# Performance work log

Measured on AMD Instinct MI355X. Metric: run time of the kernel, lower is better.

Reference implementation:

```python
import jax, jax.numpy as jnp
import numpy as np

N_NODES = 40000            # num nodes (maybe_num_nodes)
E = 2_560_000              # input edges
SENTINEL = N_NODES * N_NODES  # key for masked-out edges; sorts last; fits int32 (1.6e9 < 2^31)


def setup_inputs() -> dict:
    key = jax.random.key(0)
    k1, k2 = jax.random.split(key)
    edge_index = jax.random.randint(k1, (2, E), 0, N_NODES, dtype=jnp.int32)
    edge_attr = jax.random.uniform(k2, (E,), dtype=jnp.float32)
    t = jnp.full((1,), 0.5, dtype=jnp.float32)  # learnable threshold parameter
    return {"edge_index": edge_index, "edge_attr": edge_attr, "t": t}


def reference(edge_index, edge_attr, t):
    """Threshold mask -> symmetrize -> coalesce (sort by (row,col), sum duplicates).

    JAX has static shapes, so compaction is expressed as masking: dropped edges get
    key=SENTINEL (sorts last) and attr contribution 0. Returns padded outputs of
    fixed size 2E plus the count of valid (unique, kept) edges. Invalid slots have
    edge_index == -1 and edge_attr == 0.
    """
    row, col = edge_index[0], edge_index[1]
    mask = edge_attr <= t[0]                      # [E] bool
    # symmetrize: stack (row,col) and (col,row), duplicate attrs  -> [2E]
    r2 = jnp.concatenate([row, col])
    c2 = jnp.concatenate([col, row])
    a2 = jnp.concatenate([edge_attr, edge_attr])
    m2 = jnp.concatenate([mask, mask])
    # coalesce: linearize key = row*N + col, sort, segment-sum duplicates
    key = jnp.where(m2, r2 * N_NODES + c2, SENTINEL)   # [2E] int32
    order = jnp.argsort(key)
    key_s = key[order]
    a_s = jnp.where(m2, a2, 0.0)[order]
    E2 = key_s.shape[0]
    new_seg = jnp.concatenate([jnp.ones((1,), bool), key_s[1:] != key_s[:-1]])
    seg = jnp.cumsum(new_seg.astype(jnp.int32)) - 1    # segment id per sorted edge
    vals = jax.ops.segment_sum(a_s, seg, num_segments=E2, indices_are_sorted=True)
    uk = jnp.full((E2,), SENTINEL, dtype=key_s.dtype).at[seg].set(key_s)
    valid = uk < SENTINEL
    out_row = jnp.where(valid, uk // N_NODES, -1)
    out_col = jnp.where(valid, uk % N_NODES, -1)
    edge_index_out = jnp.stack([out_row, out_col])     # [2, 2E] padded with -1
    edge_attr_out = jnp.where(valid, vals, 0.0)        # [2E]   padded with 0
    num_edges = jnp.sum(valid.astype(jnp.int32))
    return edge_index_out, edge_attr_out, num_edges
```

## Files before the change

### kernel.cpp

```cpp
#include <hip/hip_runtime.h>
#include <stdint.h>

#define NN 40000
#define E_IN 2560000
#define E2 5120000
#define NFINE 2500
#define NSB 20
#define SB_SHIFT 11
#define FINES_PER_SB 128
#define P2_TILES 17
#define P2_TILE 8192
#define SBCAP 135168
#define CAPB 1280
#define CSTR 16
#define P1_BLOCKS 625
#define P1_THREADS 1024
#define OF_BLOCKS 625
#define OF_ITERS 8

typedef unsigned long long ull;

__global__ void k_init(int* __restrict__ sbCursor, int* __restrict__ fineCursor) {
    int tid = threadIdx.x;
    for (int f = tid; f < NFINE; f += 256) fineCursor[f * CSTR] = f * CAPB;
    if (tid < NSB) sbCursor[tid * CSTR] = tid * SBCAP;
}

__global__ void __launch_bounds__(P1_THREADS) k_part1(const int* __restrict__ ei,
                                                      const float* __restrict__ ea,
                                                      const float* __restrict__ t,
                                                      int* __restrict__ sbCursor,
                                                      ull* __restrict__ pairs1) {
    __shared__ ull staged[8192];
    __shared__ int cntO[NSB * 8];
    __shared__ int off[NSB + 1], wb[NSB * 8], gbase[NSB];
    int tid = threadIdx.x;
    int oct = (tid >> 3) & 7;
    if (tid < NSB * 8) cntO[tid] = 0;
    __syncthreads();
    float t0 = t[0];
    int i0 = blockIdx.x * 4096 + tid * 4;

    float4 a4 = *(const float4*)(ea + i0);
    int4 r4 = *(const int4*)(ei + i0);
    int4 c4 = *(const int4*)(ei + E_IN + i0);
    float av[4] = {a4.x, a4.y, a4.z, a4.w};
    int rv[4] = {r4.x, r4.y, r4.z, r4.w};
    int cv[4] = {c4.x, c4.y, c4.z, c4.w};

    ull eA[4], eB[4];
    int rkA[4], rkB[4];
    bool keep[4];
#pragma unroll
    for (int k = 0; k < 4; k++) {
        keep[k] = (av[k] <= t0);
        if (keep[k]) {
            unsigned ab = __float_as_uint(av[k]);
            eA[k] = ((ull)(unsigned)rv[k] << 48) | ((ull)(unsigned)cv[k] << 32) | ab;
            eB[k] = ((ull)(unsigned)cv[k] << 48) | ((ull)(unsigned)rv[k] << 32) | ab;
            rkA[k] = atomicAdd(&cntO[((rv[k] >> SB_SHIFT) << 3) | oct], 1);
            rkB[k] = atomicAdd(&cntO[((cv[k] >> SB_SHIFT) << 3) | oct], 1);
        }
    }
    __syncthreads();
    if (tid < NSB) {
        int s = tid;
        int c[8], tot = 0;
#pragma unroll
        for (int o = 0; o < 8; o++) { c[o] = cntO[s * 8 + o]; tot += c[o]; }
        int incl = tot;
#pragma unroll
        for (int d = 1; d < 32; d <<= 1) {
            int y = __shfl_up(incl, d, 64);
            if (s >= d) incl += y;
        }
        int o0 = incl - tot;
        off[s] = o0;
        if (s == NSB - 1) off[NSB] = incl;
        int acc = o0;
#pragma unroll
        for (int o = 0; o < 8; o++) { wb[s * 8 + o] = acc; acc += c[o]; }
        gbase[s] = atomicAdd(&sbCursor[s * CSTR], tot);
    }
    __syncthreads();
#pragma unroll
    for (int k = 0; k < 4; k++) {
        if (keep[k]) {
            staged[wb[(((int)(eA[k] >> 59)) << 3) | oct] + rkA[k]] = eA[k];
            staged[wb[(((int)(eB[k] >> 59)) << 3) | oct] + rkB[k]] = eB[k];
        }
    }
    __syncthreads();
    int total = off[NSB];
    for (int i = tid; i < total; i += P1_THREADS) {
        ull e = staged[i];
        int sb = (int)(e >> 59);
        pairs1[gbase[sb] + (i - off[sb])] = e;
    }
}

__global__ void __launch_bounds__(1024) k_part2(const int* __restrict__ sbCursor,
                                                int* __restrict__ fineCursor,
                                                const ull* __restrict__ pairs1,
                                                ull* __restrict__ pairs2) {
    int sb = blockIdx.x / P2_TILES;
    int tile = blockIdx.x % P2_TILES;
    int regionBase = sb * SBCAP;
    int len = sbCursor[sb * CSTR] - regionBase;
    if (len > SBCAP) len = SBCAP;
    int start = tile * P2_TILE;
    if (start >= len) return;
    int cntT = len - start; if (cntT > P2_TILE) cntT = P2_TILE;
    const ull* src = pairs1 + regionBase + start;

    int fineFirst = sb * FINES_PER_SB;
    int nF = NFINE - fineFirst; if (nF > FINES_PER_SB) nF = FINES_PER_SB;

    __shared__ ull staged[P2_TILE];
    __shared__ int cnt[FINES_PER_SB], off[FINES_PER_SB + 1], gbase[FINES_PER_SB], wsum2[2];
    int tid = threadIdx.x;
    if (tid < FINES_PER_SB) { cnt[tid] = 0; gbase[tid] = 0; }
    __syncthreads();

    ull e[8];
    int rk[8];
#pragma unroll
    for (int k = 0; k < 8; k++) {
        int i = tid + k * 1024;
        if (i < cntT) {
            e[k] = src[i];
            rk[k] = atomicAdd(&cnt[(int)(e[k] >> 52) & 127], 1);
        }
    }
    __syncthreads();
    int x = 0, incl = 0;
    if (tid < FINES_PER_SB) {
        x = cnt[tid];
        incl = x;
        int lane = tid & 63;
#pragma unroll
        for (int d = 1; d < 64; d <<= 1) {
            int y = __shfl_up(incl, d, 64);
            if (lane >= d) incl += y;
        }
        if (lane == 63) wsum2[tid >> 6] = incl;
    }
    __syncthreads();
    if (tid == 0) { int a = wsum2[0]; wsum2[0] = 0; wsum2[1] = a; }
    __syncthreads();
    if (tid < FINES_PER_SB) {
        off[tid] = wsum2[tid >> 6] + incl - x;
        if (tid == FINES_PER_SB - 1) off[FINES_PER_SB] = wsum2[1] + incl;
        if (tid < nF) gbase[tid] = atomicAdd(&fineCursor[(fineFirst + tid) * CSTR], x);
    }
    __syncthreads();
#pragma unroll
    for (int k = 0; k < 8; k++) {
        int i = tid + k * 1024;
        if (i < cntT) staged[off[(int)(e[k] >> 52) & 127] + rk[k]] = e[k];
    }
    __syncthreads();
    int total = off[FINES_PER_SB];
    for (int i = tid; i < total; i += 1024) {
        ull v = staged[i];
        int lb = (int)(v >> 52) & 127;
        pairs2[gbase[lb] + (i - off[lb])] = v;
    }
}

__device__ __forceinline__ void ce(ull& a, ull& b) {
    ull mn = a < b ? a : b;
    ull mx = a < b ? b : a;
    a = mn; b = mx;
}
__device__ __forceinline__ void sort8(ull* v) {
    ce(v[0],v[1]); ce(v[2],v[3]); ce(v[4],v[5]); ce(v[6],v[7]);
    ce(v[0],v[2]); ce(v[1],v[3]); ce(v[4],v[6]); ce(v[5],v[7]);
    ce(v[1],v[2]); ce(v[5],v[6]);
    ce(v[0],v[4]); ce(v[1],v[5]); ce(v[2],v[6]); ce(v[3],v[7]);
    ce(v[2],v[4]); ce(v[3],v[5]);
    ce(v[1],v[2]); ce(v[3],v[4]); ce(v[5],v[6]);
}
__device__ __forceinline__ void sort16(ull* v) {
    sort8(v); sort8(v + 8);
    ce(v[0],v[8]);  ce(v[1],v[9]);  ce(v[2],v[10]); ce(v[3],v[11]);
    ce(v[4],v[12]); ce(v[5],v[13]); ce(v[6],v[14]); ce(v[7],v[15]);
    ce(v[4],v[8]);  ce(v[5],v[9]);  ce(v[6],v[10]); ce(v[7],v[11]);
    ce(v[2],v[4]);  ce(v[3],v[5]);  ce(v[6],v[8]);  ce(v[7],v[9]);  ce(v[10],v[12]); ce(v[11],v[13]);
    ce(v[1],v[2]);  ce(v[3],v[4]);  ce(v[5],v[6]);  ce(v[7],v[8]);  ce(v[9],v[10]);  ce(v[11],v[12]); ce(v[13],v[14]);
}

__global__ void __launch_bounds__(512) k_sortrows(const int* __restrict__ fineCursor,
                                                  ull* __restrict__ pairs2,
                                                  int* __restrict__ uniqueCount) {
    int b = blockIdx.x;
    int base = b * CAPB;
    int n = fineCursor[b * CSTR] - base;
    if (n > CAPB) n = CAPB;
    __shared__ ull d[CAPB];
    __shared__ int cnt[512], off[512], wsum[8], ucnt[16], ubase[16];
    int tid = threadIdx.x;
    int lane = tid & 63;
    cnt[tid] = 0;
    __syncthreads();

    ull e[3]; int rk[3], sbk[3];
#pragma unroll
    for (int k = 0; k < 3; k++) {
        int i = tid + k * 512;
        if (i < n) {
            e[k] = pairs2[base + i];
            sbk[k] = (int)(e[k] >> 43) & 511;
            rk[k] = atomicAdd(&cnt[sbk[k]], 1);
        }
    }
    __syncthreads();

    int x = cnt[tid];
    int incl = x;
#pragma unroll
    for (int dlt = 1; dlt < 64; dlt <<= 1) {
        int y = __shfl_up(incl, dlt, 64);
        if (lane >= dlt) incl += y;
    }
    if (lane == 63) wsum[tid >> 6] = incl;
    __syncthreads();
    if (tid == 0) {
        int a = 0;
        for (int w = 0; w < 8; w++) { int tt = wsum[w]; wsum[w] = a; a += tt; }
    }
    __syncthreads();
    off[tid] = wsum[tid >> 6] + incl - x;
    __syncthreads();

#pragma unroll
    for (int k = 0; k < 3; k++) {
        int i = tid + k * 512;
        if (i < n) d[off[sbk[k]] + rk[k]] = e[k];
    }
    __syncthreads();

    int cn = cnt[tid]; if (cn > 16) cn = 16;
    int o0 = off[tid];
    ull v[16];
    bool big = __any(cn > 8);
    if (!big) {
#pragma unroll
        for (int k = 0; k < 8; k++) v[k] = (k < cn) ? d[o0 + k] : ~0ull;
        sort8(v);
    } else {
#pragma unroll
        for (int k = 0; k < 16; k++) v[k] = (k < cn) ? d[o0 + k] : ~0ull;
        sort16(v);
    }

    int uc = (cn > 0) ? 1 : 0;
#pragma unroll
    for (int k = 1; k < 16; k++)
        if (k < cn && (unsigned)(v[k] >> 32) != (unsigned)(v[k - 1] >> 32)) uc++;

    int uincl = uc;
#pragma unroll
    for (int dlt = 1; dlt < 64; dlt <<= 1) {
        int y = __shfl_up(uincl, dlt, 64);
        if (lane >= dlt) uincl += y;
    }
    int rowTot0 = __shfl(uincl, 31, 64);
    int rr = tid >> 5;
    int rowOff = uincl - uc - ((lane >= 32) ? rowTot0 : 0);
    if (lane == 31) ucnt[rr] = uincl;
    if (lane == 63) ucnt[rr] = uincl - rowTot0;
    __syncthreads();
    if (tid == 0) {
        int acc = 0;
        for (int s = 0; s < 16; s++) { ubase[s] = acc; acc += ucnt[s]; }
        uniqueCount[b] = acc;
    }
    __syncthreads();

    if (cn > 0) {
        ull* dst = pairs2 + base + ubase[rr] + rowOff;
        unsigned curKey = (unsigned)(v[0] >> 32);
        float curSum = __uint_as_float((unsigned)v[0]);
        int em = 0;
#pragma unroll
        for (int k = 1; k < 16; k++) {
            if (k < cn) {
                unsigned key = (unsigned)(v[k] >> 32);
                float a = __uint_as_float((unsigned)v[k]);
                if (key == curKey) {
                    curSum += a;
                } else {
                    dst[em] = ((ull)curKey << 32) | __float_as_uint(curSum);
                    em++;
                    curKey = key; curSum = a;
                }
            }
        }
        dst[em] = ((ull)curKey << 32) | __float_as_uint(curSum);
    }
}

__global__ void __launch_bounds__(256) k_outfill(const int* __restrict__ uniqueCount,
                                                 const ull* __restrict__ pairs2,
                                                 float* __restrict__ out) {
    __shared__ int sOB[NFINE + 1];
    __shared__ int wsum[4];
    int tid = threadIdx.x, lane = tid & 63, w = tid >> 6;
    int v10[10]; int sum = 0;
    int s0 = tid * 10;
#pragma unroll
    for (int k = 0; k < 10; k++) {
        int i = s0 + k;
        int x = (i < NFINE) ? uniqueCount[i] : 0;
        v10[k] = sum;
        sum += x;
    }
    int incl = sum;
#pragma unroll
    for (int d = 1; d < 64; d <<= 1) {
        int y = __shfl_up(incl, d, 64);
        if (lane >= d) incl += y;
    }
    if (lane == 63) wsum[w] = incl;
    __syncthreads();
    if (tid == 0) { int a = 0; for (int i = 0; i < 4; i++) { int t2 = wsum[i]; wsum[i] = a; a += t2; } }
    __syncthreads();
    int tbase = wsum[w] + incl - sum;
#pragma unroll
    for (int k = 0; k < 10; k++) {
        int i = s0 + k;
        if (i < NFINE) sOB[i] = tbase + v10[k];
    }
    if (tid == 255) sOB[NFINE] = tbase + sum;
    __syncthreads();
    int T = sOB[NFINE];
    if (blockIdx.x == 0 && tid == 0) out[(size_t)3 * E2] = (float)T;

    int lo = 0;
    bool searched = false;
    for (int it = 0; it < OF_ITERS; it++) {
        int tile = blockIdx.x * OF_ITERS + it;
        int j0 = (tile * 256 + tid) * 4;
        float rr[4], cc[4], aa[4];
        if (j0 < T && !searched) {
            int hi = NFINE;
            while (hi - lo > 1) {
                int mid = (lo + hi) >> 1;
                if (sOB[mid] <= j0) lo = mid; else hi = mid;
            }
            searched = true;
        }
#pragma unroll
        for (int k = 0; k < 4; k++) {
            int j = j0 + k;
            if (j < T) {
                while (lo < NFINE - 1 && sOB[lo + 1] <= j) lo++;
                ull e = pairs2[lo * CAPB + (j - sOB[lo])];
                rr[k] = (float)(int)(e >> 48);
                cc[k] = (float)(int)((e >> 32) & 0xFFFF);
                aa[k] = __uint_as_float((unsigned)(e & 0xFFFFFFFFu));
            } else { rr[k] = -1.0f; cc[k] = -1.0f; aa[k] = 0.0f; }
        }
        *(float4*)(out + j0)          = make_float4(rr[0], rr[1], rr[2], rr[3]);
        *(float4*)(out + E2 + j0)     = make_float4(cc[0], cc[1], cc[2], cc[3]);
        *(float4*)(out + 2 * E2 + j0) = make_float4(aa[0], aa[1], aa[2], aa[3]);
    }
}

extern "C" void kernel_launch(void* const* d_in, const int* in_sizes, int n_in,
                              void* d_out, int out_size, void* d_ws, size_t ws_size,
                              hipStream_t stream) {
    const int*   ei = (const int*)d_in[0];
    const float* ea = (const float*)d_in[1];
    const float* t  = (const float*)d_in[2];
    float* out = (float*)d_out;

    int* sbCursor    = (int*)d_ws;
    int* fineCursor  = sbCursor + NSB * CSTR;
    int* uniqueCount = fineCursor + NFINE * CSTR;
    ull* pairs2 = (ull*)(((uintptr_t)(uniqueCount + NFINE) + 15) & ~(uintptr_t)15);

    ull* pairs1 = (ull*)d_out;

    k_init<<<1, 256, 0, stream>>>(sbCursor, fineCursor);
    k_part1<<<P1_BLOCKS, P1_THREADS, 0, stream>>>(ei, ea, t, sbCursor, pairs1);
    k_part2<<<NSB * P2_TILES, 1024, 0, stream>>>(sbCursor, fineCursor, pairs1, pairs2);
    k_sortrows<<<NFINE, 512, 0, stream>>>(fineCursor, pairs2, uniqueCount);
    k_outfill<<<OF_BLOCKS, 256, 0, stream>>>(uniqueCount, pairs2, out);
}
```

Before: 159.5 us.

## Fuse output compaction into row sort via decoupled look-back scan

The row-sort kernel now keeps coalesced entries in shared memory and finds its global output offset with a decoupled look-back prefix scan over per-block state flags. It then writes row, col and attr directly to the output, which removes the separate outfill pass that re-read pairs2 and binary-searched block offsets. A small pad-fill kernel writes the -1/0 tail and the count. Part2 is also retuned to 512 threads with 4096-element tiles. The look-back adds spin-waiting between blocks and relies on blocks being scheduled roughly in order for forward progress.

```diff
diff --git a/kernel.cpp b/kernel.cpp
--- a/kernel.cpp
+++ b/kernel.cpp
@@ -8,21 +8,24 @@
 #define NSB 20
 #define SB_SHIFT 11
 #define FINES_PER_SB 128
-#define P2_TILES 17
-#define P2_TILE 8192
+#define P2_TILES 33
+#define P2_TILE 4096
+#define P2_THREADS 512
 #define SBCAP 135168
 #define CAPB 1280
 #define CSTR 16
 #define P1_BLOCKS 625
 #define P1_THREADS 1024
-#define OF_BLOCKS 625
-#define OF_ITERS 8
 
 typedef unsigned long long ull;
 
-__global__ void k_init(int* __restrict__ sbCursor, int* __restrict__ fineCursor) {
+__global__ void k_init(int* __restrict__ sbCursor, int* __restrict__ fineCursor,
+                       ull* __restrict__ state) {
     int tid = threadIdx.x;
-    for (int f = tid; f < NFINE; f += 256) fineCursor[f * CSTR] = f * CAPB;
+    for (int f = tid; f < NFINE; f += 256) {
+        fineCursor[f * CSTR] = f * CAPB;
+        state[f] = 0;
+    }
     if (tid < NSB) sbCursor[tid * CSTR] = tid * SBCAP;
 }
 
@@ -99,10 +102,10 @@
     }
 }
 
-__global__ void __launch_bounds__(1024) k_part2(const int* __restrict__ sbCursor,
-                                                int* __restrict__ fineCursor,
-                                                const ull* __restrict__ pairs1,
-                                                ull* __restrict__ pairs2) {
+__global__ void __launch_bounds__(P2_THREADS) k_part2(const int* __restrict__ sbCursor,
+                                                      int* __restrict__ fineCursor,
+                                                      const ull* __restrict__ pairs1,
+                                                      ull* __restrict__ pairs2) {
     int sb = blockIdx.x / P2_TILES;
     int tile = blockIdx.x % P2_TILES;
     int regionBase = sb * SBCAP;
@@ -126,7 +129,7 @@
     int rk[8];
 #pragma unroll
     for (int k = 0; k < 8; k++) {
-        int i = tid + k * 1024;
+        int i = tid + k * P2_THREADS;
         if (i < cntT) {
             e[k] = src[i];
             rk[k] = atomicAdd(&cnt[(int)(e[k] >> 52) & 127], 1);
@@ -156,12 +159,12 @@
     __syncthreads();
 #pragma unroll
     for (int k = 0; k < 8; k++) {
-        int i = tid + k * 1024;
+        int i = tid + k * P2_THREADS;
         if (i < cntT) staged[off[(int)(e[k] >> 52) & 127] + rk[k]] = e[k];
     }
     __syncthreads();
     int total = off[FINES_PER_SB];
-    for (int i = tid; i < total; i += 1024) {
+    for (int i = tid; i < total; i += P2_THREADS) {
         ull v = staged[i];
         int lb = (int)(v >> 52) & 127;
         pairs2[gbase[lb] + (i - off[lb])] = v;
@@ -191,16 +194,20 @@
 }
 
 __global__ void __launch_bounds__(512) k_sortrows(const int* __restrict__ fineCursor,
-                                                  ull* __restrict__ pairs2,
-                                                  int* __restrict__ uniqueCount) {
+                                                  const ull* __restrict__ pairs2,
+                                                  ull* __restrict__ state,
+                                                  int* __restrict__ uniqueTotal,
+                                                  float* __restrict__ out) {
     int b = blockIdx.x;
     int base = b * CAPB;
     int n = fineCursor[b * CSTR] - base;
     if (n > CAPB) n = CAPB;
     __shared__ ull d[CAPB];
     __shared__ int cnt[512], off[512], wsum[8], ucnt[16], ubase[16];
+    __shared__ int sGB, sTot;
     int tid = threadIdx.x;
     int lane = tid & 63;
+    int wave = tid >> 6;
     cnt[tid] = 0;
     __syncthreads();
 
@@ -274,12 +281,50 @@
     if (tid == 0) {
         int acc = 0;
         for (int s = 0; s < 16; s++) { ubase[s] = acc; acc += ucnt[s]; }
-        uniqueCount[b] = acc;
-    }
-    __syncthreads();
+        sTot = acc;
+        if (b == 0) {
+            sGB = 0;
+            __hip_atomic_store(&state[0], (2ULL << 32) | (unsigned)acc,
+                               __ATOMIC_RELEASE, __HIP_MEMORY_SCOPE_AGENT);
+        } else {
+            __hip_atomic_store(&state[b], (1ULL << 32) | (unsigned)acc,
+                               __ATOMIC_RELEASE, __HIP_MEMORY_SCOPE_AGENT);
+        }
+    }
+    __syncthreads();
+
+    if (b > 0 && wave == 0) {
+        int winBase = b - 1;
+        int running = 0;
+        while (true) {
+            int idx = winBase - lane;
+            ull s = (idx >= 0)
+                ? __hip_atomic_load(&state[idx], __ATOMIC_ACQUIRE, __HIP_MEMORY_SCOPE_AGENT)
+                : (2ULL << 32);
+            int flag = (int)(s >> 32);
+            ull ballInv = __ballot(flag == 0);
+            ull ballPre = __ballot(flag == 2);
+            int fi = ballInv ? __builtin_ctzll(ballInv) : 64;
+            int fp = ballPre ? __builtin_ctzll(ballPre) : 64;
+            if (fi < fp) { __builtin_amdgcn_s_sleep(1); continue; }
+            int lim = (fp < 64) ? fp : 63;
+            int contrib = (lane <= lim) ? (int)(unsigned)(s & 0xFFFFFFFFu) : 0;
+#pragma unroll
+            for (int d2 = 1; d2 < 64; d2 <<= 1) contrib += __shfl_xor(contrib, d2, 64);
+            running += contrib;
+            if (fp < 64) break;
+            winBase -= 64;
+        }
+        if (lane == 0) {
+            sGB = running;
+            __hip_atomic_store(&state[b], (2ULL << 32) | (unsigned)(running + sTot),
+                               __ATOMIC_RELEASE, __HIP_MEMORY_SCOPE_AGENT);
+            if (b == NFINE - 1) *uniqueTotal = running + sTot;
+        }
+    }
 
     if (cn > 0) {
-        ull* dst = pairs2 + base + ubase[rr] + rowOff;
+        int dstoff = ubase[rr] + rowOff;
         unsigned curKey = (unsigned)(v[0] >> 32);
         float curSum = __uint_as_float((unsigned)v[0]);
         int em = 0;
@@ -291,80 +336,41 @@
                 if (key == curKey) {
                     curSum += a;
                 } else {
-                    dst[em] = ((ull)curKey << 32) | __float_as_uint(curSum);
+                    d[dstoff + em] = ((ull)curKey << 32) | __float_as_uint(curSum);
                     em++;
                     curKey = key; curSum = a;
                 }
             }
         }
-        dst[em] = ((ull)curKey << 32) | __float_as_uint(curSum);
-    }
-}
-
-__global__ void __launch_bounds__(256) k_outfill(const int* __restrict__ uniqueCount,
-                                                 const ull* __restrict__ pairs2,
+        d[dstoff + em] = ((ull)curKey << 32) | __float_as_uint(curSum);
+    }
+    __syncthreads();
+
+    int tot = sTot, gb = sGB;
+    for (int j = tid; j < tot; j += 512) {
+        ull ee = d[j];
+        out[gb + j]          = (float)(int)(ee >> 48);
+        out[E2 + gb + j]     = (float)(int)((ee >> 32) & 0xFFFF);
+        out[2 * E2 + gb + j] = __uint_as_float((unsigned)(ee & 0xFFFFFFFFu));
+    }
+}
+
+__global__ void __launch_bounds__(256) k_padfill(const int* __restrict__ uniqueTotal,
                                                  float* __restrict__ out) {
-    __shared__ int sOB[NFINE + 1];
-    __shared__ int wsum[4];
-    int tid = threadIdx.x, lane = tid & 63, w = tid >> 6;
-    int v10[10]; int sum = 0;
-    int s0 = tid * 10;
-#pragma unroll
-    for (int k = 0; k < 10; k++) {
-        int i = s0 + k;
-        int x = (i < NFINE) ? uniqueCount[i] : 0;
-        v10[k] = sum;
-        sum += x;
-    }
-    int incl = sum;
-#pragma unroll
-    for (int d = 1; d < 64; d <<= 1) {
-        int y = __shfl_up(incl, d, 64);
-        if (lane >= d) incl += y;
-    }
-    if (lane == 63) wsum[w] = incl;
-    __syncthreads();
-    if (tid == 0) { int a = 0; for (int i = 0; i < 4; i++) { int t2 = wsum[i]; wsum[i] = a; a += t2; } }
-    __syncthreads();
-    int tbase = wsum[w] + incl - sum;
-#pragma unroll
-    for (int k = 0; k < 10; k++) {
-        int i = s0 + k;
-        if (i < NFINE) sOB[i] = tbase + v10[k];
-    }
-    if (tid == 255) sOB[NFINE] = tbase + sum;
-    __syncthreads();
-    int T = sOB[NFINE];
-    if (blockIdx.x == 0 && tid == 0) out[(size_t)3 * E2] = (float)T;
-
-    int lo = 0;
-    bool searched = false;
-    for (int it = 0; it < OF_ITERS; it++) {
-        int tile = blockIdx.x * OF_ITERS + it;
-        int j0 = (tile * 256 + tid) * 4;
-        float rr[4], cc[4], aa[4];
-        if (j0 < T && !searched) {
-            int hi = NFINE;
-            while (hi - lo > 1) {
-                int mid = (lo + hi) >> 1;
-                if (sOB[mid] <= j0) lo = mid; else hi = mid;
-            }
-            searched = true;
-        }
-#pragma unroll
-        for (int k = 0; k < 4; k++) {
-            int j = j0 + k;
-            if (j < T) {
-                while (lo < NFINE - 1 && sOB[lo + 1] <= j) lo++;
-                ull e = pairs2[lo * CAPB + (j - sOB[lo])];
-                rr[k] = (float)(int)(e >> 48);
-                cc[k] = (float)(int)((e >> 32) & 0xFFFF);
-                aa[k] = __uint_as_float((unsigned)(e & 0xFFFFFFFFu));
-            } else { rr[k] = -1.0f; cc[k] = -1.0f; aa[k] = 0.0f; }
-        }
-        *(float4*)(out + j0)          = make_float4(rr[0], rr[1], rr[2], rr[3]);
-        *(float4*)(out + E2 + j0)     = make_float4(cc[0], cc[1], cc[2], cc[3]);
-        *(float4*)(out + 2 * E2 + j0) = make_float4(aa[0], aa[1], aa[2], aa[3]);
+    int T = *uniqueTotal;
+    int j0 = (blockIdx.x * 256 + threadIdx.x) * 4;
+    if (blockIdx.x == 0 && threadIdx.x == 0) out[(size_t)3 * E2] = (float)T;
+    if (j0 + 4 <= T) return;
+    if (j0 >= T) {
+        float4 m1 = make_float4(-1.f, -1.f, -1.f, -1.f);
+        float4 z  = make_float4(0.f, 0.f, 0.f, 0.f);
+        *(float4*)(out + j0)          = m1;
+        *(float4*)(out + E2 + j0)     = m1;
+        *(float4*)(out + 2 * E2 + j0) = z;
+    } else {
+        for (int j = T; j < j0 + 4; j++) {
+            out[j] = -1.f; out[E2 + j] = -1.f; out[2 * E2 + j] = 0.f;
+        }
     }
 }
 
@@ -378,14 +384,15 @@
 
     int* sbCursor    = (int*)d_ws;
     int* fineCursor  = sbCursor + NSB * CSTR;
-    int* uniqueCount = fineCursor + NFINE * CSTR;
-    ull* pairs2 = (ull*)(((uintptr_t)(uniqueCount + NFINE) + 15) & ~(uintptr_t)15);
+    int* uniqueTotal = fineCursor + NFINE * CSTR;
+    ull* state  = (ull*)(((uintptr_t)(uniqueTotal + 16) + 15) & ~(uintptr_t)15);
+    ull* pairs2 = state + NFINE;
 
     ull* pairs1 = (ull*)d_out;
 
-    k_init<<<1, 256, 0, stream>>>(sbCursor, fineCursor);
+    k_init<<<1, 256, 0, stream>>>(sbCursor, fineCursor, state);
     k_part1<<<P1_BLOCKS, P1_THREADS, 0, stream>>>(ei, ea, t, sbCursor, pairs1);
-    k_part2<<<NSB * P2_TILES, 1024, 0, stream>>>(sbCursor, fineCursor, pairs1, pairs2);
-    k_sortrows<<<NFINE, 512, 0, stream>>>(fineCursor, pairs2, uniqueCount);
-    k_outfill<<<OF_BLOCKS, 256, 0, stream>>>(uniqueCount, pairs2, out);
-}
+    k_part2<<<NSB * P2_TILES, P2_THREADS, 0, stream>>>(sbCursor, fineCursor, pairs1, pairs2);
+    k_sortrows<<<NFINE, 512, 0, stream>>>(fineCursor, pairs2, state, uniqueTotal, out);
+    k_padfill<<<E2 / 1024, 256, 0, stream>>>(uniqueTotal, out);
+}
```

Result: slower. 337.1 us (+111.4%).
